# Optimization experiments

Measured on AMD Instinct MI355X. Metric: run time of the kernel, lower is better.

Reference implementation:

```python
import jax, jax.numpy as jnp
import numpy as np

N_NODES = 50000
N_EDGES = 800000
D_IN = 256
D_HID = 128
NUM_LAYERS = 6
ALPHA = 0.1
THETA = 0.5
EPS = 1e-5  # BatchNorm1d default eps


def setup_inputs() -> dict:
    key = jax.random.key(0)
    ks = jax.random.split(key, 6)
    x = jax.random.normal(ks[0], (N_NODES, D_IN), dtype=jnp.float32)
    edge_index = jax.random.randint(ks[1], (2, N_EDGES), 0, N_NODES)
    # GCNConv(D_IN, D_HID): weight + bias
    W_lin = jax.random.normal(ks[2], (D_IN, D_HID), dtype=jnp.float32) / np.sqrt(D_IN).astype(np.float32)
    b_lin = jnp.zeros((D_HID,), jnp.float32)
    # GCN2Conv weight1 per layer (shared_weights=True -> only weight1, no bias)
    W1s = jax.random.normal(ks[3], (NUM_LAYERS - 1, D_HID, D_HID), dtype=jnp.float32) / np.sqrt(D_HID).astype(np.float32)
    # BatchNorm1d affine params per intermediate layer
    bn_gamma = jnp.ones((NUM_LAYERS - 2, D_HID), jnp.float32)
    bn_beta = jnp.zeros((NUM_LAYERS - 2, D_HID), jnp.float32)
    return {"x": x, "edge_index": edge_index, "W_lin": W_lin, "b_lin": b_lin,
            "W1s": W1s, "bn_gamma": bn_gamma, "bn_beta": bn_beta}


def _gcn_conv(x, W, b, edge_index):
    # PyG GCNConv: transform, add self-loops, D^{-1/2}(A+I)D^{-1/2} aggregation.
    n = x.shape[0]
    xw = x @ W  # [N, D_HID]
    loop = jnp.arange(n)
    src = jnp.concatenate([edge_index[0], loop])
    dst = jnp.concatenate([edge_index[1], loop])
    deg = jax.ops.segment_sum(jnp.ones(src.shape, xw.dtype), dst, num_segments=n)
    dinv = jax.lax.rsqrt(jnp.maximum(deg, 1.0))  # deg >= 1 thanks to self loops
    w = dinv[src] * dinv[dst]  # [E+N]
    return jax.ops.segment_sum(xw[src] * w[:, None], dst, num_segments=n) + b


def _gcn2_conv(z, x0, W1, edge_index, beta):
    # GCN2Conv with normalize=False, shared_weights=True:
    # h = (1-alpha)*sum_{j->i} z_j + alpha*x0 ; out = (1-beta)*h + beta*(h @ W1)
    n = z.shape[0]
    agg = jax.ops.segment_sum(z[edge_index[0]], edge_index[1], num_segments=n)
    h = (1.0 - ALPHA) * agg + ALPHA * x0
    return (1.0 - beta) * h + beta * (h @ W1)


def _batchnorm(z, gamma, beta_p):
    # training-mode BatchNorm1d over the node dimension (biased variance)
    mu = jnp.mean(z, axis=0)
    var = jnp.var(z, axis=0)
    return (z - mu) * jax.lax.rsqrt(var + EPS) * gamma + beta_p


def reference(x, edge_index, W_lin, b_lin, W1s, bn_gamma, bn_beta):
    z = _gcn_conv(x, W_lin, b_lin, edge_index)
    x0 = z
    n_convs = NUM_LAYERS - 1
    # GCN2Conv layer index l = i+1 -> beta_l = log(theta/l + 1)
    betas = [float(np.log(THETA / (i + 1) + 1.0)) for i in range(n_convs)]
    for i in range(n_convs):  # dropout=0.0 -> identity, omitted
        z = _gcn2_conv(z, x0, W1s[i], edge_index, betas[i])
        if i < n_convs - 1:
            z = _batchnorm(z, bn_gamma[i], bn_beta[i])
            z = jax.nn.relu(z)
    return z
```

## Files before the change

kernel.cpp:

```cpp
#include <hip/hip_runtime.h>
#include <math.h>

#define N_NODES 50000
#define N_EDGES 800000
#define D_IN 256
#define D_HID 128
#define ALPHA 0.1f
#define EPS 1e-5f

#define NBUCK 391
#define EPB 4096
#define NBLK 196

typedef __attribute__((ext_vector_type(8))) short bf16x8;
typedef __attribute__((ext_vector_type(4))) float f32x4;

static __device__ __forceinline__ unsigned short f2bf(float f) {
    unsigned int x = __float_as_uint(f);
    return (unsigned short)((x + 0x7fffu + ((x >> 16) & 1u)) >> 16);
}
static __device__ __forceinline__ float blo(unsigned int v) {
    return __uint_as_float(v << 16);
}
static __device__ __forceinline__ float bhi(unsigned int v) {
    return __uint_as_float(v & 0xffff0000u);
}
static __device__ __forceinline__ void unpack8(uint4 u, float* f) {
    f[0] = blo(u.x); f[1] = bhi(u.x);
    f[2] = blo(u.y); f[3] = bhi(u.y);
    f[4] = blo(u.z); f[5] = bhi(u.z);
    f[6] = blo(u.w); f[7] = bhi(u.w);
}

__global__ __launch_bounds__(256) void k_hist(const int* __restrict__ dst,
                                              int* __restrict__ hist, int e) {
    __shared__ int h[NBUCK];
    int t = threadIdx.x;
    for (int i = t; i < NBUCK; i += 256) h[i] = 0;
    __syncthreads();
    int base = blockIdx.x * EPB;
    int lim = e - base;
    if (lim > EPB) lim = EPB;
    for (int i = t; i < lim; i += 256) atomicAdd(&h[dst[base + i] >> 7], 1);
    __syncthreads();
    for (int i = t; i < NBUCK; i += 256) hist[blockIdx.x * NBUCK + i] = h[i];
}

__global__ __launch_bounds__(256) void k_bkscan(const int* __restrict__ hist,
                                                int* __restrict__ offsT, int* __restrict__ btot) {
    __shared__ int sh[256];
    int b = blockIdx.x;
    int t = threadIdx.x;
    int v = (t < NBLK) ? hist[t * NBUCK + b] : 0;
    sh[t] = v;
    __syncthreads();
    for (int ofs = 1; ofs < 256; ofs <<= 1) {
        int y = (t >= ofs) ? sh[t - ofs] : 0;
        __syncthreads();
        sh[t] += y;
        __syncthreads();
    }
    if (t < NBLK) offsT[b * NBLK + t] = sh[t] - v;
    if (t == 255) btot[b] = sh[255];
}

__global__ __launch_bounds__(512) void k_bbase(const int* __restrict__ btot,
                                               int* __restrict__ bbase, int* __restrict__ rp) {
    __shared__ int sh[512];
    int t = threadIdx.x;
    int v = (t < NBUCK) ? btot[t] : 0;
    sh[t] = v;
    __syncthreads();
    for (int ofs = 1; ofs < 512; ofs <<= 1) {
        int y = (t >= ofs) ? sh[t - ofs] : 0;
        __syncthreads();
        sh[t] += y;
        __syncthreads();
    }
    if (t < NBUCK) bbase[t] = sh[t] - v;
    if (t == 0) rp[N_NODES] = N_EDGES;
}

__global__ __launch_bounds__(256) void k_scatter(const int* __restrict__ src,
                                                 const int* __restrict__ dst,
                                                 const int* __restrict__ offsT,
                                                 const int* __restrict__ bbase,
                                                 unsigned int* __restrict__ buck, int e) {
    __shared__ int h[NBUCK];
    int t = threadIdx.x;
    for (int i = t; i < NBUCK; i += 256) h[i] = 0;
    __syncthreads();
    int base = blockIdx.x * EPB;
    int lim = e - base;
    if (lim > EPB) lim = EPB;
    for (int i = t; i < lim; i += 256) {
        int d = dst[base + i];
        int s = src[base + i];
        int b = d >> 7;
        int lp = atomicAdd(&h[b], 1);
        int pos = bbase[b] + offsT[b * NBLK + blockIdx.x] + lp;
        buck[pos] = (unsigned int)s | ((unsigned int)(d & 127) << 16);
    }
}

__global__ __launch_bounds__(256) void k_csr(const unsigned int* __restrict__ buck,
                                             const int* __restrict__ bbase,
                                             const int* __restrict__ btot,
                                             int* __restrict__ rp, float* __restrict__ dinv,
                                             unsigned short* __restrict__ cs) {
    __shared__ int dcnt[128];
    __shared__ int doff[128];
    int b = blockIdx.x;
    int t = threadIdx.x;
    if (t < 128) dcnt[t] = 0;
    __syncthreads();
    int base = bbase[b];
    int tot = btot[b];
    for (int i = t; i < tot; i += 256) {
        unsigned int v = buck[base + i];
        atomicAdd(&dcnt[(v >> 16) & 127], 1);
    }
    __syncthreads();
    if (t < 128) doff[t] = dcnt[t];
    __syncthreads();
    for (int ofs = 1; ofs < 128; ofs <<= 1) {
        int y = 0;
        if (t < 128 && t >= ofs) y = doff[t - ofs];
        __syncthreads();
        if (t < 128) doff[t] += y;
        __syncthreads();
    }
    int gd0 = b << 7;
    if (t < 128) {
        int ex = doff[t] - dcnt[t];
        if (gd0 + t < N_NODES) {
            rp[gd0 + t] = base + ex;
            dinv[gd0 + t] = rsqrtf((float)(dcnt[t] + 1));
        }
        dcnt[t] = ex;
    }
    __syncthreads();
    for (int i = t; i < tot; i += 256) {
        unsigned int v = buck[base + i];
        int p = atomicAdd(&dcnt[(v >> 16) & 127], 1);
        cs[base + p] = (unsigned short)(v & 0xffffu);
    }
}

__global__ __launch_bounds__(256) void k_cast_x(const float4* __restrict__ x, ushort2* __restrict__ xb,
                                                int n4) {
    int i = blockIdx.x * 256 + threadIdx.x;
    if (i < n4) {
        float4 v = x[i];
        ushort2 a;
        a.x = f2bf(v.x); a.y = f2bf(v.y);
        ushort2 b;
        b.x = f2bf(v.z); b.y = f2bf(v.w);
        xb[i * 2] = a;
        xb[i * 2 + 1] = b;
    }
}

__global__ __launch_bounds__(256) void k_prep_w(const float* __restrict__ W_lin,
                                                const float* __restrict__ W1s,
                                                unsigned short* __restrict__ Wlt,
                                                unsigned short* __restrict__ Wt) {
    int idx = blockIdx.x * 256 + threadIdx.x;
    if (idx < 128 * 256) {
        int c = idx >> 8, k = idx & 255;
        Wlt[idx] = f2bf(W_lin[k * 128 + c]);
    } else {
        int j = idx - 128 * 256;
        if (j < 5 * 128 * 128) {
            int l = j >> 14;
            int rem = j & 16383;
            int c = rem >> 7, k = rem & 127;
            float bet = logf(0.5f / (float)(l + 1) + 1.0f);
            float v = bet * W1s[l * 16384 + k * 128 + c];
            if (c == k) v += 1.0f - bet;
            Wt[j] = f2bf(v);
        }
    }
}

template <int K>
__global__ __launch_bounds__(256) void k_mgemm(const unsigned short* __restrict__ A,
                                               const unsigned short* __restrict__ Bt,
                                               unsigned short* __restrict__ outb, int M) {
    __shared__ short lds[2 * 128 * 136];
    short* As = lds;
    short* Bs = lds + 128 * 136;

    int t = threadIdx.x;
    int lane = t & 63;
    int wave = t >> 6;
    int wr = wave >> 1, wc = wave & 1;
    int row0 = blockIdx.x * 128;

    f32x4 acc[4][4];
#pragma unroll
    for (int m = 0; m < 4; ++m)
#pragma unroll
        for (int n = 0; n < 4; ++n) acc[m][n] = (f32x4){0.f, 0.f, 0.f, 0.f};

    int sr = t >> 1;
    int sh = t & 1;

    for (int k0 = 0; k0 < K; k0 += 128) {
        {
            int gr = row0 + sr;
            uint4 zero = {0, 0, 0, 0};
            const uint4* gp = (const uint4*)(A + (size_t)gr * K + k0 + sh * 64);
#pragma unroll
            for (int u = 0; u < 8; ++u) {
                uint4 v = (gr < M) ? gp[u] : zero;
                *(uint4*)(As + sr * 136 + sh * 64 + u * 8) = v;
            }
        }
        {
            const uint4* gp = (const uint4*)(Bt + (size_t)sr * K + k0 + sh * 64);
#pragma unroll
            for (int u = 0; u < 8; ++u) {
                *(uint4*)(Bs + sr * 136 + sh * 64 + u * 8) = gp[u];
            }
        }
        __syncthreads();

#pragma unroll
        for (int ks = 0; ks < 4; ++ks) {
            bf16x8 af[4], bfr[4];
#pragma unroll
            for (int m = 0; m < 4; ++m)
                af[m] = *(const bf16x8*)(As + (wr * 64 + m * 16 + (lane & 15)) * 136 + ks * 32 + (lane >> 4) * 8);
#pragma unroll
            for (int n = 0; n < 4; ++n)
                bfr[n] = *(const bf16x8*)(Bs + (wc * 64 + n * 16 + (lane & 15)) * 136 + ks * 32 + (lane >> 4) * 8);
#pragma unroll
            for (int m = 0; m < 4; ++m)
#pragma unroll
                for (int n = 0; n < 4; ++n)
                    acc[m][n] = __builtin_amdgcn_mfma_f32_16x16x32_bf16(af[m], bfr[n], acc[m][n], 0, 0, 0);
        }
        __syncthreads();
    }

    short* Z = lds;
#pragma unroll
    for (int m = 0; m < 4; ++m)
#pragma unroll
        for (int n = 0; n < 4; ++n)
#pragma unroll
            for (int r = 0; r < 4; ++r) {
                int rl = wr * 64 + m * 16 + (lane >> 4) * 4 + r;
                int cl = wc * 64 + n * 16 + (lane & 15);
                Z[rl * 136 + cl] = (short)f2bf(acc[m][n][r]);
            }
    __syncthreads();
    int gr = row0 + sr;
    if (gr < M) {
#pragma unroll
        for (int u = 0; u < 8; ++u)
            *(uint4*)(outb + (size_t)gr * 128 + sh * 64 + u * 8) = *(uint4*)(Z + sr * 136 + sh * 64 + u * 8);
    }
}

template <int MODE>
__global__ __launch_bounds__(256) void k_lgemm(const unsigned short* __restrict__ A,
                                               const unsigned short* __restrict__ Bt,
                                               unsigned short* __restrict__ outb,
                                               float* __restrict__ outf,
                                               float* __restrict__ bn_s, float* __restrict__ bn_q,
                                               int M) {
    __shared__ short As[128 * 136];
    int t = threadIdx.x;
    int lane = t & 63;
    int wave = t >> 6;
    int wr = wave >> 1, wc = wave & 1;
    int row0 = blockIdx.x * 128;

    bf16x8 bfr[4][4];
#pragma unroll
    for (int ks = 0; ks < 4; ++ks)
#pragma unroll
        for (int n = 0; n < 4; ++n)
            bfr[ks][n] = *(const bf16x8*)(Bt + (size_t)(wc * 64 + n * 16 + (lane & 15)) * 128 + ks * 32 + (lane >> 4) * 8);

    int sr = t >> 1, sh = t & 1;
    {
        int gr = row0 + sr;
        uint4 zero = {0, 0, 0, 0};
        const uint4* gp = (const uint4*)(A + (size_t)gr * 128 + sh * 64);
#pragma unroll
        for (int u = 0; u < 8; ++u) {
            uint4 v = (gr < M) ? gp[u] : zero;
            *(uint4*)(As + sr * 136 + sh * 64 + u * 8) = v;
        }
    }
    __syncthreads();

    f32x4 acc[4][4];
#pragma unroll
    for (int m = 0; m < 4; ++m)
#pragma unroll
        for (int n = 0; n < 4; ++n) acc[m][n] = (f32x4){0.f, 0.f, 0.f, 0.f};

#pragma unroll
    for (int ks = 0; ks < 4; ++ks) {
        bf16x8 af[4];
#pragma unroll
        for (int m = 0; m < 4; ++m)
            af[m] = *(const bf16x8*)(As + (wr * 64 + m * 16 + (lane & 15)) * 136 + ks * 32 + (lane >> 4) * 8);
#pragma unroll
        for (int m = 0; m < 4; ++m)
#pragma unroll
            for (int n = 0; n < 4; ++n)
                acc[m][n] = __builtin_amdgcn_mfma_f32_16x16x32_bf16(af[m], bfr[ks][n], acc[m][n], 0, 0, 0);
    }

    if (MODE == 1) {
        float sum[4] = {0.f, 0.f, 0.f, 0.f}, sq[4] = {0.f, 0.f, 0.f, 0.f};
#pragma unroll
        for (int n = 0; n < 4; ++n)
#pragma unroll
            for (int m = 0; m < 4; ++m)
#pragma unroll
                for (int r = 0; r < 4; ++r) {
                    float v = acc[m][n][r];
                    sum[n] += v;
                    sq[n] += v * v;
                }
#pragma unroll
        for (int n = 0; n < 4; ++n) {
            sum[n] += __shfl_xor(sum[n], 16);
            sum[n] += __shfl_xor(sum[n], 32);
            sq[n] += __shfl_xor(sq[n], 16);
            sq[n] += __shfl_xor(sq[n], 32);
        }
        if (lane < 16) {
#pragma unroll
            for (int n = 0; n < 4; ++n) {
                int col = wc * 64 + n * 16 + lane;
                atomicAdd(&bn_s[col], sum[n]);
                atomicAdd(&bn_q[col], sq[n]);
            }
        }
    }

    if (MODE == 2) {
#pragma unroll
        for (int m = 0; m < 4; ++m)
#pragma unroll
            for (int n = 0; n < 4; ++n)
#pragma unroll
                for (int r = 0; r < 4; ++r) {
                    int gr = row0 + wr * 64 + m * 16 + (lane >> 4) * 4 + r;
                    int cl = wc * 64 + n * 16 + (lane & 15);
                    if (gr < M) outf[(size_t)gr * 128 + cl] = acc[m][n][r];
                }
    } else {
        __syncthreads();
        short* Z = As;
#pragma unroll
        for (int m = 0; m < 4; ++m)
#pragma unroll
            for (int n = 0; n < 4; ++n)
#pragma unroll
                for (int r = 0; r < 4; ++r) {
                    int rl = wr * 64 + m * 16 + (lane >> 4) * 4 + r;
                    int cl = wc * 64 + n * 16 + (lane & 15);
                    Z[rl * 136 + cl] = (short)f2bf(acc[m][n][r]);
                }
        __syncthreads();
        int gr = row0 + sr;
        if (gr < M) {
#pragma unroll
            for (int u = 0; u < 8; ++u)
                *(uint4*)(outb + (size_t)gr * 128 + sh * 64 + u * 8) = *(uint4*)(Z + sr * 136 + sh * 64 + u * 8);
        }
    }
}

template <int MODE>
__global__ __launch_bounds__(256) void k_agg(const uint4* __restrict__ src4,
                                             const uint4* __restrict__ x04,
                                             const int* __restrict__ rp,
                                             const unsigned short* __restrict__ cs,
                                             const float* __restrict__ dinv,
                                             const float* __restrict__ b_lin,
                                             const float* __restrict__ st,
                                             uint4* __restrict__ dst4,
                                             float* __restrict__ bns, int n) {
    if (blockIdx.x == 0) bns[threadIdx.x] = 0.f;

    int wgl = (blockIdx.x * 256 + threadIdx.x) >> 6;
    int n0 = wgl * 4;
    if (n0 >= n) return;
    int lane = threadIdx.x & 63;
    int q = lane >> 4;
    int c = lane & 15;

    int bidx = n0 + ((lane < 4) ? lane : 4);
    if (bidx > n) bidx = n;
    int rr = rp[bidx];
    int e0 = __shfl(rr, 0);
    int e1 = __shfl(rr, 1);
    int e2 = __shfl(rr, 2);
    int e3 = __shfl(rr, 3);
    int e4 = __shfl(rr, 4);
    int eb[5] = {e0, e1, e2, e3, e4};

    float dnv = 0.f;
    if (MODE == 0) {
        int di = n0 + ((lane < 4) ? lane : 3);
        if (di >= n) di = n - 1;
        dnv = dinv[di];
    }

    float sc[8], tc[8];
    if (MODE == 2) {
        float4 s0 = ((const float4*)st)[c * 2];
        float4 s1 = ((const float4*)st)[c * 2 + 1];
        float4 t0 = ((const float4*)st)[32 + c * 2];
        float4 t1 = ((const float4*)st)[32 + c * 2 + 1];
        sc[0] = s0.x; sc[1] = s0.y; sc[2] = s0.z; sc[3] = s0.w;
        sc[4] = s1.x; sc[5] = s1.y; sc[6] = s1.z; sc[7] = s1.w;
        tc[0] = t0.x; tc[1] = t0.y; tc[2] = t0.z; tc[3] = t0.w;
        tc[4] = t1.x; tc[5] = t1.y; tc[6] = t1.z; tc[7] = t1.w;
    }

    float acc[4][8];
#pragma unroll
    for (int k = 0; k < 4; ++k)
#pragma unroll
        for (int i = 0; i < 8; ++i) acc[k][i] = 0.f;

#define ACC1(K_, vv, ww)                                                   \
    {                                                                      \
        float f_[8];                                                       \
        unpack8(vv, f_);                                                   \
        if (MODE == 0) {                                                   \
            _Pragma("unroll") for (int i_ = 0; i_ < 8; ++i_)               \
                acc[K_][i_] = fmaf(ww, f_[i_], acc[K_][i_]);               \
        } else if (MODE == 1) {                                            \
            _Pragma("unroll") for (int i_ = 0; i_ < 8; ++i_)               \
                acc[K_][i_] = fmaf(ww, f_[i_], acc[K_][i_]);               \
        } else {                                                           \
            _Pragma("unroll") for (int i_ = 0; i_ < 8; ++i_)               \
                acc[K_][i_] = fmaf(ww, fmaxf(fmaf(sc[i_], f_[i_], tc[i_]), 0.f), acc[K_][i_]); \
        }                                                                  \
    }

    int total = e4 - e0;
    for (int chunk = 0; chunk < total; chunk += 64) {
        int cnt = total - chunk;
        if (cnt > 64) cnt = 64;
        int li = (lane < cnt) ? lane : (cnt - 1);
        int myi = (int)cs[e0 + chunk + li];
        float myw = (MODE == 0) ? dinv[myi] : 0.f;

#pragma unroll
        for (int k = 0; k < 4; ++k) {
            int lo = eb[k] - e0 - chunk;
            int hi = eb[k + 1] - e0 - chunk;
            if (lo < 0) lo = 0;
            if (hi > cnt) hi = cnt;
            float dnk = (MODE == 0) ? __shfl(dnv, k) : 0.f;
            for (int j = lo; j < hi; j += 16) {
                if (j + 16 <= hi) {
                    int j0 = j + q, j1 = j + 4 + q, j2 = j + 8 + q, j3 = j + 12 + q;
                    int i0 = __shfl(myi, j0);
                    int i1 = __shfl(myi, j1);
                    int i2 = __shfl(myi, j2);
                    int i3 = __shfl(myi, j3);
                    uint4 v0 = src4[(size_t)i0 * 16 + c];
                    uint4 v1 = src4[(size_t)i1 * 16 + c];
                    uint4 v2 = src4[(size_t)i2 * 16 + c];
                    uint4 v3 = src4[(size_t)i3 * 16 + c];
                    float w0 = 1.f, w1 = 1.f, w2 = 1.f, w3 = 1.f;
                    if (MODE == 0) {
                        w0 = __shfl(myw, j0) * dnk;
                        w1 = __shfl(myw, j1) * dnk;
                        w2 = __shfl(myw, j2) * dnk;
                        w3 = __shfl(myw, j3) * dnk;
                    }
                    ACC1(k, v0, w0);
                    ACC1(k, v1, w1);
                    ACC1(k, v2, w2);
                    ACC1(k, v3, w3);
                } else {
#pragma unroll
                    for (int b4 = 0; b4 < 4; ++b4) {
                        int jj = j + b4 * 4 + q;
                        if (j + b4 * 4 >= hi) break;
                        bool act = jj < hi;
                        int js = act ? jj : (hi - 1);
                        int i0 = __shfl(myi, js);
                        uint4 v0 = src4[(size_t)i0 * 16 + c];
                        float m = act ? 1.f : 0.f;
                        float w0 = m;
                        if (MODE == 0) w0 = __shfl(myw, js) * dnk * m;
                        ACC1(k, v0, w0);
                    }
                }
            }
        }
    }
#undef ACC1

#pragma unroll
    for (int k = 0; k < 4; ++k) {
        int node = n0 + k;
        if (node >= n) break;
#pragma unroll
        for (int i = 0; i < 8; ++i) {
            acc[k][i] += __shfl_xor(acc[k][i], 16);
            acc[k][i] += __shfl_xor(acc[k][i], 32);
        }
        if (lane < 16) {
            float res[8];
            if (MODE == 0) {
                uint4 sv = src4[(size_t)node * 16 + c];
                float fs[8];
                unpack8(sv, fs);
                float dnk = __shfl(dnv, k);
                float w2 = dnk * dnk;
                float4 b0 = ((const float4*)b_lin)[c * 2];
                float4 b1 = ((const float4*)b_lin)[c * 2 + 1];
                float bb[8] = {b0.x, b0.y, b0.z, b0.w, b1.x, b1.y, b1.z, b1.w};
#pragma unroll
                for (int i = 0; i < 8; ++i) res[i] = fmaf(w2, fs[i], acc[k][i]) + bb[i];
            } else {
                uint4 xv = x04[(size_t)node * 16 + c];
                float fx[8];
                unpack8(xv, fx);
#pragma unroll
                for (int i = 0; i < 8; ++i) res[i] = fmaf(ALPHA, fx[i], (1.0f - ALPHA) * acc[k][i]);
            }
            uint4 o;
            o.x = (unsigned int)f2bf(res[0]) | ((unsigned int)f2bf(res[1]) << 16);
            o.y = (unsigned int)f2bf(res[2]) | ((unsigned int)f2bf(res[3]) << 16);
            o.z = (unsigned int)f2bf(res[4]) | ((unsigned int)f2bf(res[5]) << 16);
            o.w = (unsigned int)f2bf(res[6]) | ((unsigned int)f2bf(res[7]) << 16);
            dst4[(size_t)node * 16 + c] = o;
        }
    }
}

__global__ void k_bn_fin(const float* __restrict__ bn_s, const float* __restrict__ bn_q,
                         const float* __restrict__ gamma, const float* __restrict__ betap,
                         float* __restrict__ st, int n) {
    int c = threadIdx.x;
    float inv_n = 1.0f / (float)n;
    float mu = bn_s[c] * inv_n;
    float var = bn_q[c] * inv_n - mu * mu;
    var = fmaxf(var, 0.f);
    float s = gamma[c] * rsqrtf(var + EPS);
    st[c] = s;
    st[128 + c] = betap[c] - mu * s;
}

extern "C" void kernel_launch(void* const* d_in, const int* in_sizes, int n_in,
                              void* d_out, int out_size, void* d_ws, size_t ws_size,
                              hipStream_t stream) {
    const float* x = (const float*)d_in[0];
    const int* ei = (const int*)d_in[1];
    const float* W_lin = (const float*)d_in[2];
    const float* b_lin = (const float*)d_in[3];
    const float* W1s = (const float*)d_in[4];
    const float* gam = (const float*)d_in[5];
    const float* betp = (const float*)d_in[6];
    float* out = (float*)d_out;

    char* ws = (char*)d_ws;
    size_t off = 0;
    auto alloc = [&](size_t b) { size_t p = off; off = (off + b + 255) & ~(size_t)255; return p; };
    int* rp = (int*)(ws + alloc((size_t)(N_NODES + 1) * 4));
    unsigned short* cs = (unsigned short*)(ws + alloc((size_t)N_EDGES * 2));
    float* dinv = (float*)(ws + alloc((size_t)N_NODES * 4));
    int* hist = (int*)(ws + alloc((size_t)NBLK * NBUCK * 4));
    int* offsT = (int*)(ws + alloc((size_t)NBUCK * NBLK * 4));
    int* btot = (int*)(ws + alloc((size_t)NBUCK * 4));
    int* bbase = (int*)(ws + alloc((size_t)NBUCK * 4));
    unsigned int* buck = (unsigned int*)(ws + alloc((size_t)N_EDGES * 4));
    unsigned short* xb = (unsigned short*)(ws + alloc((size_t)N_NODES * D_IN * 2));
    unsigned short* xwb = (unsigned short*)(ws + alloc((size_t)N_NODES * D_HID * 2));
    unsigned short* x0b = (unsigned short*)(ws + alloc((size_t)N_NODES * D_HID * 2));
    unsigned short* zb = (unsigned short*)(ws + alloc((size_t)N_NODES * D_HID * 2));
    unsigned short* hb = (unsigned short*)(ws + alloc((size_t)N_NODES * D_HID * 2));
    unsigned short* Wlt = (unsigned short*)(ws + alloc((size_t)128 * 256 * 2));
    unsigned short* Wt = (unsigned short*)(ws + alloc((size_t)5 * 128 * 128 * 2));
    float* bns = (float*)(ws + alloc(256 * 4));
    float* st = (float*)(ws + alloc(256 * 4));

    const int ggrid = (N_NODES + 127) / 128;
    const int agrid = (N_NODES + 15) / 16;

    k_hist<<<NBLK, 256, 0, stream>>>(ei + N_EDGES, hist, N_EDGES);
    k_bkscan<<<NBUCK, 256, 0, stream>>>(hist, offsT, btot);
    k_bbase<<<1, 512, 0, stream>>>(btot, bbase, rp);
    k_scatter<<<NBLK, 256, 0, stream>>>(ei, ei + N_EDGES, offsT, bbase, buck, N_EDGES);
    k_csr<<<NBUCK, 256, 0, stream>>>(buck, bbase, btot, rp, dinv, cs);

    k_cast_x<<<(N_NODES * D_IN / 4 + 255) / 256, 256, 0, stream>>>((const float4*)x, (ushort2*)xb,
                                                                   N_NODES * D_IN / 4);
    k_prep_w<<<(128 * 256 + 5 * 128 * 128 + 255) / 256, 256, 0, stream>>>(W_lin, W1s, Wlt, Wt);

    k_mgemm<D_IN><<<ggrid, 256, 0, stream>>>(xb, Wlt, xwb, N_NODES);
    k_agg<0><<<agrid, 256, 0, stream>>>((const uint4*)xwb, nullptr, rp, cs, dinv, b_lin,
                                        nullptr, (uint4*)x0b, bns, N_NODES);

    for (int i = 0; i < 5; ++i) {
        const unsigned short* zsrc = (i == 0) ? x0b : zb;
        if (i == 0)
            k_agg<1><<<agrid, 256, 0, stream>>>((const uint4*)zsrc, (const uint4*)x0b,
                                                rp, cs, nullptr, nullptr, nullptr,
                                                (uint4*)hb, bns, N_NODES);
        else
            k_agg<2><<<agrid, 256, 0, stream>>>((const uint4*)zsrc, (const uint4*)x0b,
                                                rp, cs, nullptr, nullptr, st,
                                                (uint4*)hb, bns, N_NODES);
        const unsigned short* W1 = Wt + (size_t)i * 128 * 128;
        if (i < 4) {
            k_lgemm<1><<<ggrid, 256, 0, stream>>>(hb, W1, zb, nullptr, bns, bns + 128, N_NODES);
            k_bn_fin<<<1, 128, 0, stream>>>(bns, bns + 128, gam + (size_t)i * 128,
                                            betp + (size_t)i * 128, st, N_NODES);
        } else {
            k_lgemm<2><<<ggrid, 256, 0, stream>>>(hb, W1, nullptr, out, nullptr, nullptr, N_NODES);
        }
    }
}
```

Baseline: 456.1 us.

## Assign one node per block with two wavefronts splitting feature columns in aggregation

The SpMM aggregation kernel used to give each 64-lane wavefront four destination nodes, with 16 lanes covering the 128 bf16 columns and 4 edges handled at once. It now launches one 128-thread block per node, and each of the two wavefronts covers half of the columns with 8 lanes times 8 edge slots. The aim is to balance uneven node degrees and raise the number of gathers in flight per node. In exchange the grid grows to 50000 small blocks, each wavefront only loads 128-byte row halves, and every block repeats the index loads and shuffles.

```diff
diff --git a/kernel.cpp b/kernel.cpp
--- a/kernel.cpp
+++ b/kernel.cpp
@@ -381,7 +381,7 @@
 }
 
 template <int MODE>
-__global__ __launch_bounds__(256) void k_agg(const uint4* __restrict__ src4,
+__global__ __launch_bounds__(128) void k_agg(const uint4* __restrict__ src4,
                                              const uint4* __restrict__ x04,
                                              const int* __restrict__ rp,
                                              const unsigned short* __restrict__ cs,
@@ -390,159 +390,144 @@
                                              const float* __restrict__ st,
                                              uint4* __restrict__ dst4,
                                              float* __restrict__ bns, int n) {
-    if (blockIdx.x == 0) bns[threadIdx.x] = 0.f;
-
-    int wgl = (blockIdx.x * 256 + threadIdx.x) >> 6;
-    int n0 = wgl * 4;
-    if (n0 >= n) return;
+    if (blockIdx.x == 0) {
+        bns[threadIdx.x] = 0.f;
+        bns[threadIdx.x + 128] = 0.f;
+    }
+    int node = blockIdx.x;
+    if (node >= n) return;
+    int half = threadIdx.x >> 6;
     int lane = threadIdx.x & 63;
-    int q = lane >> 4;
-    int c = lane & 15;
-
-    int bidx = n0 + ((lane < 4) ? lane : 4);
-    if (bidx > n) bidx = n;
-    int rr = rp[bidx];
-    int e0 = __shfl(rr, 0);
-    int e1 = __shfl(rr, 1);
-    int e2 = __shfl(rr, 2);
-    int e3 = __shfl(rr, 3);
-    int e4 = __shfl(rr, 4);
-    int eb[5] = {e0, e1, e2, e3, e4};
-
-    float dnv = 0.f;
-    if (MODE == 0) {
-        int di = n0 + ((lane < 4) ? lane : 3);
-        if (di >= n) di = n - 1;
-        dnv = dinv[di];
-    }
+    int q = lane >> 3;
+    int c = lane & 7;
+    int col4 = half * 8 + c;
+
+    int start = __builtin_amdgcn_readfirstlane(rp[node]);
+    int end = __builtin_amdgcn_readfirstlane(rp[node + 1]);
 
     float sc[8], tc[8];
     if (MODE == 2) {
-        float4 s0 = ((const float4*)st)[c * 2];
-        float4 s1 = ((const float4*)st)[c * 2 + 1];
-        float4 t0 = ((const float4*)st)[32 + c * 2];
-        float4 t1 = ((const float4*)st)[32 + c * 2 + 1];
+        float4 s0 = ((const float4*)st)[col4 * 2];
+        float4 s1 = ((const float4*)st)[col4 * 2 + 1];
+        float4 t0 = ((const float4*)st)[32 + col4 * 2];
+        float4 t1 = ((const float4*)st)[32 + col4 * 2 + 1];
         sc[0] = s0.x; sc[1] = s0.y; sc[2] = s0.z; sc[3] = s0.w;
         sc[4] = s1.x; sc[5] = s1.y; sc[6] = s1.z; sc[7] = s1.w;
         tc[0] = t0.x; tc[1] = t0.y; tc[2] = t0.z; tc[3] = t0.w;
         tc[4] = t1.x; tc[5] = t1.y; tc[6] = t1.z; tc[7] = t1.w;
     }
-
-    float acc[4][8];
-#pragma unroll
-    for (int k = 0; k < 4; ++k)
-#pragma unroll
-        for (int i = 0; i < 8; ++i) acc[k][i] = 0.f;
-
-#define ACC1(K_, vv, ww)                                                   \
+    float dn = (MODE == 0) ? dinv[node] : 0.f;
+
+    float acc[8];
+#pragma unroll
+    for (int i = 0; i < 8; ++i) acc[i] = 0.f;
+
+#define ACCW(vv, ww)                                                       \
     {                                                                      \
         float f_[8];                                                       \
         unpack8(vv, f_);                                                   \
-        if (MODE == 0) {                                                   \
+        if (MODE == 2) {                                                   \
             _Pragma("unroll") for (int i_ = 0; i_ < 8; ++i_)               \
-                acc[K_][i_] = fmaf(ww, f_[i_], acc[K_][i_]);               \
-        } else if (MODE == 1) {                                            \
-            _Pragma("unroll") for (int i_ = 0; i_ < 8; ++i_)               \
-                acc[K_][i_] = fmaf(ww, f_[i_], acc[K_][i_]);               \
+                acc[i_] = fmaf(ww, fmaxf(fmaf(sc[i_], f_[i_], tc[i_]), 0.f), acc[i_]); \
         } else {                                                           \
             _Pragma("unroll") for (int i_ = 0; i_ < 8; ++i_)               \
-                acc[K_][i_] = fmaf(ww, fmaxf(fmaf(sc[i_], f_[i_], tc[i_]), 0.f), acc[K_][i_]); \
+                acc[i_] = fmaf(ww, f_[i_], acc[i_]);                       \
         }                                                                  \
     }
-
-    int total = e4 - e0;
-    for (int chunk = 0; chunk < total; chunk += 64) {
-        int cnt = total - chunk;
+#define ACCP(vv)                                                           \
+    {                                                                      \
+        float f_[8];                                                       \
+        unpack8(vv, f_);                                                   \
+        if (MODE == 2) {                                                   \
+            _Pragma("unroll") for (int i_ = 0; i_ < 8; ++i_)               \
+                acc[i_] += fmaxf(fmaf(sc[i_], f_[i_], tc[i_]), 0.f);       \
+        } else {                                                           \
+            _Pragma("unroll") for (int i_ = 0; i_ < 8; ++i_)               \
+                acc[i_] += f_[i_];                                         \
+        }                                                                  \
+    }
+
+    for (int base = start; base < end; base += 64) {
+        int cnt = end - base;
         if (cnt > 64) cnt = 64;
         int li = (lane < cnt) ? lane : (cnt - 1);
-        int myi = (int)cs[e0 + chunk + li];
+        int myi = (int)cs[base + li];
         float myw = (MODE == 0) ? dinv[myi] : 0.f;
 
-#pragma unroll
-        for (int k = 0; k < 4; ++k) {
-            int lo = eb[k] - e0 - chunk;
-            int hi = eb[k + 1] - e0 - chunk;
-            if (lo < 0) lo = 0;
-            if (hi > cnt) hi = cnt;
-            float dnk = (MODE == 0) ? __shfl(dnv, k) : 0.f;
-            for (int j = lo; j < hi; j += 16) {
-                if (j + 16 <= hi) {
-                    int j0 = j + q, j1 = j + 4 + q, j2 = j + 8 + q, j3 = j + 12 + q;
-                    int i0 = __shfl(myi, j0);
-                    int i1 = __shfl(myi, j1);
-                    int i2 = __shfl(myi, j2);
-                    int i3 = __shfl(myi, j3);
-                    uint4 v0 = src4[(size_t)i0 * 16 + c];
-                    uint4 v1 = src4[(size_t)i1 * 16 + c];
-                    uint4 v2 = src4[(size_t)i2 * 16 + c];
-                    uint4 v3 = src4[(size_t)i3 * 16 + c];
-                    float w0 = 1.f, w1 = 1.f, w2 = 1.f, w3 = 1.f;
-                    if (MODE == 0) {
-                        w0 = __shfl(myw, j0) * dnk;
-                        w1 = __shfl(myw, j1) * dnk;
-                        w2 = __shfl(myw, j2) * dnk;
-                        w3 = __shfl(myw, j3) * dnk;
-                    }
-                    ACC1(k, v0, w0);
-                    ACC1(k, v1, w1);
-                    ACC1(k, v2, w2);
-                    ACC1(k, v3, w3);
-                } else {
-#pragma unroll
-                    for (int b4 = 0; b4 < 4; ++b4) {
-                        int jj = j + b4 * 4 + q;
-                        if (j + b4 * 4 >= hi) break;
-                        bool act = jj < hi;
-                        int js = act ? jj : (hi - 1);
-                        int i0 = __shfl(myi, js);
-                        uint4 v0 = src4[(size_t)i0 * 16 + c];
-                        float m = act ? 1.f : 0.f;
-                        float w0 = m;
-                        if (MODE == 0) w0 = __shfl(myw, js) * dnk * m;
-                        ACC1(k, v0, w0);
-                    }
-                }
+        int j = 0;
+        for (; j + 16 <= cnt; j += 16) {
+            int j0 = j + q, j1 = j + 8 + q;
+            int i0 = __shfl(myi, j0);
+            int i1 = __shfl(myi, j1);
+            uint4 v0 = src4[(size_t)i0 * 16 + col4];
+            uint4 v1 = src4[(size_t)i1 * 16 + col4];
+            if (MODE == 0) {
+                float w0 = __shfl(myw, j0) * dn;
+                float w1 = __shfl(myw, j1) * dn;
+                ACCW(v0, w0);
+                ACCW(v1, w1);
+            } else {
+                ACCP(v0);
+                ACCP(v1);
             }
         }
-    }
-#undef ACC1
-
-#pragma unroll
-    for (int k = 0; k < 4; ++k) {
-        int node = n0 + k;
-        if (node >= n) break;
-#pragma unroll
-        for (int i = 0; i < 8; ++i) {
-            acc[k][i] += __shfl_xor(acc[k][i], 16);
-            acc[k][i] += __shfl_xor(acc[k][i], 32);
-        }
-        if (lane < 16) {
-            float res[8];
+        for (; j + 8 <= cnt; j += 8) {
+            int j0 = j + q;
+            int i0 = __shfl(myi, j0);
+            uint4 v0 = src4[(size_t)i0 * 16 + col4];
             if (MODE == 0) {
-                uint4 sv = src4[(size_t)node * 16 + c];
-                float fs[8];
-                unpack8(sv, fs);
-                float dnk = __shfl(dnv, k);
-                float w2 = dnk * dnk;
-                float4 b0 = ((const float4*)b_lin)[c * 2];
-                float4 b1 = ((const float4*)b_lin)[c * 2 + 1];
-                float bb[8] = {b0.x, b0.y, b0.z, b0.w, b1.x, b1.y, b1.z, b1.w};
-#pragma unroll
-                for (int i = 0; i < 8; ++i) res[i] = fmaf(w2, fs[i], acc[k][i]) + bb[i];
+                float w0 = __shfl(myw, j0) * dn;
+                ACCW(v0, w0);
             } else {
-                uint4 xv = x04[(size_t)node * 16 + c];
-                float fx[8];
-                unpack8(xv, fx);
-#pragma unroll
-                for (int i = 0; i < 8; ++i) res[i] = fmaf(ALPHA, fx[i], (1.0f - ALPHA) * acc[k][i]);
+                ACCP(v0);
             }
-            uint4 o;
-            o.x = (unsigned int)f2bf(res[0]) | ((unsigned int)f2bf(res[1]) << 16);
-            o.y = (unsigned int)f2bf(res[2]) | ((unsigned int)f2bf(res[3]) << 16);
-            o.z = (unsigned int)f2bf(res[4]) | ((unsigned int)f2bf(res[5]) << 16);
-            o.w = (unsigned int)f2bf(res[6]) | ((unsigned int)f2bf(res[7]) << 16);
-            dst4[(size_t)node * 16 + c] = o;
-        }
+        }
+        if (j < cnt) {
+            int jj = j + q;
+            bool act = jj < cnt;
+            int js = act ? jj : (cnt - 1);
+            int i0 = __shfl(myi, js);
+            uint4 v0 = src4[(size_t)i0 * 16 + col4];
+            float m = act ? 1.f : 0.f;
+            float w0 = (MODE == 0) ? (__shfl(myw, js) * dn * m) : m;
+            ACCW(v0, w0);
+        }
+    }
+#undef ACCW
+#undef ACCP
+
+#pragma unroll
+    for (int i = 0; i < 8; ++i) {
+        acc[i] += __shfl_xor(acc[i], 8);
+        acc[i] += __shfl_xor(acc[i], 16);
+        acc[i] += __shfl_xor(acc[i], 32);
+    }
+
+    if (lane < 8) {
+        float res[8];
+        if (MODE == 0) {
+            uint4 sv = src4[(size_t)node * 16 + col4];
+            float fs[8];
+            unpack8(sv, fs);
+            float w2 = dn * dn;
+            float4 b0 = ((const float4*)b_lin)[col4 * 2];
+            float4 b1 = ((const float4*)b_lin)[col4 * 2 + 1];
+            float bb[8] = {b0.x, b0.y, b0.z, b0.w, b1.x, b1.y, b1.z, b1.w};
+#pragma unroll
+            for (int i = 0; i < 8; ++i) res[i] = fmaf(w2, fs[i], acc[i]) + bb[i];
+        } else {
+            uint4 xv = x04[(size_t)node * 16 + col4];
+            float fx[8];
+            unpack8(xv, fx);
+#pragma unroll
+            for (int i = 0; i < 8; ++i) res[i] = fmaf(ALPHA, fx[i], (1.0f - ALPHA) * acc[i]);
+        }
+        uint4 o;
+        o.x = (unsigned int)f2bf(res[0]) | ((unsigned int)f2bf(res[1]) << 16);
+        o.y = (unsigned int)f2bf(res[2]) | ((unsigned int)f2bf(res[3]) << 16);
+        o.z = (unsigned int)f2bf(res[4]) | ((unsigned int)f2bf(res[5]) << 16);
+        o.w = (unsigned int)f2bf(res[6]) | ((unsigned int)f2bf(res[7]) << 16);
+        dst4[(size_t)node * 16 + col4] = o;
     }
 }
 
@@ -593,7 +578,7 @@
     float* st = (float*)(ws + alloc(256 * 4));
 
     const int ggrid = (N_NODES + 127) / 128;
-    const int agrid = (N_NODES + 15) / 16;
+    const int agrid = N_NODES;
 
     k_hist<<<NBLK, 256, 0, stream>>>(ei + N_EDGES, hist, N_EDGES);
     k_bkscan<<<NBUCK, 256, 0, stream>>>(hist, offsT, btot);
@@ -606,17 +591,17 @@
     k_prep_w<<<(128 * 256 + 5 * 128 * 128 + 255) / 256, 256, 0, stream>>>(W_lin, W1s, Wlt, Wt);
 
     k_mgemm<D_IN><<<ggrid, 256, 0, stream>>>(xb, Wlt, xwb, N_NODES);
-    k_agg<0><<<agrid, 256, 0, stream>>>((const uint4*)xwb, nullptr, rp, cs, dinv, b_lin,
+    k_agg<0><<<agrid, 128, 0, stream>>>((const uint4*)xwb, nullptr, rp, cs, dinv, b_lin,
                                         nullptr, (uint4*)x0b, bns, N_NODES);
 
     for (int i = 0; i < 5; ++i) {
         const unsigned short* zsrc = (i == 0) ? x0b : zb;
         if (i == 0)
-            k_agg<1><<<agrid, 256, 0, stream>>>((const uint4*)zsrc, (const uint4*)x0b,
+            k_agg<1><<<agrid, 128, 0, stream>>>((const uint4*)zsrc, (const uint4*)x0b,
                                                 rp, cs, nullptr, nullptr, nullptr,
                                                 (uint4*)hb, bns, N_NODES);
         else
-            k_agg<2><<<agrid, 256, 0, stream>>>((const uint4*)zsrc, (const uint4*)x0b,
+            k_agg<2><<<agrid, 128, 0, stream>>>((const uint4*)zsrc, (const uint4*)x0b,
                                                 rp, cs, nullptr, nullptr, st,
                                                 (uint4*)hb, bns, N_NODES);
         const unsigned short* W1 = Wt + (size_t)i * 128 * 128;
```

Measured after the change: 448.4 us. Within noise of the previous version (-1.7%).
